# Kernel optimization log

Hardware: AMD Instinct MI355X
Metric: run time of the kernel (lower is better)

Reference implementation:

```python
import jax, jax.numpy as jnp
import numpy as np

H = 256       # lstm_hidden_size
B = 64        # batch
L = 128       # sequence length
LABEL = 128   # slot label size


def setup_inputs() -> dict:
    key = jax.random.key(0)
    ks = jax.random.split(key, 8)
    s = 1.0 / np.sqrt(H)  # torch LSTM/Linear uniform init scale
    return {
        "x": jax.random.normal(ks[0], (B, L, 2 * H), jnp.float32),
        "hi": jax.random.normal(ks[1], (B, L, 2 * H), jnp.float32),
        "W_ih": jax.random.uniform(ks[2], (4 * H, 5 * H), jnp.float32, -s, s),
        "W_hh": jax.random.uniform(ks[3], (4 * H, H), jnp.float32, -s, s),
        "b_ih": jax.random.uniform(ks[4], (4 * H,), jnp.float32, -s, s),
        "b_hh": jax.random.uniform(ks[5], (4 * H,), jnp.float32, -s, s),
        "W_fc": jax.random.uniform(ks[6], (LABEL, H), jnp.float32, -s, s),
        "b_fc": jax.random.uniform(ks[7], (LABEL,), jnp.float32, -s, s),
    }


def reference(x, hi, W_ih, W_hh, b_ih, b_hh, W_fc, b_fc):
    # dropout_rate = 0.0 -> dropout is identity.
    h_dim = W_hh.shape[1]
    bias = b_ih + b_hh  # (4H,)

    # x cat hi: (B, L, 4H) -> time-major (L, B, 4H)
    feats = jnp.transpose(jnp.concatenate([x, hi], axis=-1), (1, 0, 2))

    def cell(hc, inp):
        # PyTorch feeds (batch,1,5H) into a seq-major LSTM, so each batch
        # element is one recurrent step with batch-size 1.
        h, c = hc  # (H,), (H,)
        g = inp @ W_ih.T + h @ W_hh.T + bias  # (4H,)
        i, f, gg, o = jnp.split(g, 4)
        i = jax.nn.sigmoid(i)
        f = jax.nn.sigmoid(f)
        gg = jnp.tanh(gg)
        o = jax.nn.sigmoid(o)
        c_new = f * c + i * gg
        h_new = o * jnp.tanh(c_new)
        return (h_new, c_new), h_new

    def step(carry, x_t):
        # x_t: (B, 4H); out_prev: (B, H) = previous timestep's LSTM outputs
        h, c, out_prev = carry
        inp = jnp.concatenate([x_t, out_prev], axis=-1)  # (B, 5H)
        (h, c), outs = jax.lax.scan(cell, (h, c), inp)   # scan over batch dim
        return (h, c, outs), outs

    h0 = jnp.zeros((h_dim,), x.dtype)
    c0 = jnp.zeros((h_dim,), x.dtype)
    out0 = jnp.zeros((x.shape[0], h_dim), x.dtype)  # dec_init_out

    (_, _, _), all_out = jax.lax.scan(step, (h0, c0, out0), feats)  # (L, B, H)
    output = jnp.transpose(all_out, (1, 0, 2))  # (B, L, H)
    return output @ W_fc.T + b_fc  # (B, L, LABEL)
```

## Files before the change

kernel.cpp:

```cpp
#include <hip/hip_runtime.h>
#include <math.h>

#define H    256
#define BB   64
#define LL   128
#define LBL  128
#define NSTEP (BB*LL)
#define GDIM (4*H)
#define KDIM (4*H)
#define W5   (5*H)
#define NWG  16
#define NROW (NSTEP + 64)

typedef unsigned long long ull;

#define SW(j) ((j) + ((j) >> 4))

__global__ void k_init(ull* __restrict__ HT)
{
    const int r = blockIdx.x;
    const int e = threadIdx.x;
    HT[(ull)r * H + e] = ((ull)(unsigned)r << 32);
}

__global__ __launch_bounds__(256) void k_pre(const float* __restrict__ x,
                                             const float* __restrict__ hi,
                                             const float* __restrict__ Wih,
                                             const float* __restrict__ bih,
                                             const float* __restrict__ bhh,
                                             _Float16* __restrict__ PREh)
{
    const int nb = blockIdx.x;
    const int t  = blockIdx.y;
    const int tid = threadIdx.x;
    const int tm = tid >> 4, tn = tid & 15;

    __shared__ float As[16][68];
    __shared__ float Bs[16][68];

    const int lm  = tid >> 2;
    const int lk4 = (tid & 3) * 4;

    float acc[4][4];
#pragma unroll
    for (int i = 0; i < 4; i++)
#pragma unroll
        for (int j = 0; j < 4; j++) acc[i][j] = 0.f;

    for (int j0 = 0; j0 < KDIM; j0 += 16) {
        const int j = j0 + lk4;
        float4 av;
        if (j < 512) av = *(const float4*)(x  + ((size_t)lm * LL + t) * 512 + j);
        else         av = *(const float4*)(hi + ((size_t)lm * LL + t) * 512 + (j - 512));
        float4 bv = *(const float4*)(Wih + (size_t)(nb * 64 + lm) * W5 + j);

        __syncthreads();
        As[lk4 + 0][lm] = av.x; As[lk4 + 1][lm] = av.y;
        As[lk4 + 2][lm] = av.z; As[lk4 + 3][lm] = av.w;
        Bs[lk4 + 0][lm] = bv.x; Bs[lk4 + 1][lm] = bv.y;
        Bs[lk4 + 2][lm] = bv.z; Bs[lk4 + 3][lm] = bv.w;
        __syncthreads();

#pragma unroll
        for (int kk = 0; kk < 16; kk++) {
            float4 a = *(const float4*)&As[kk][tm << 2];
            float4 b = *(const float4*)&Bs[kk][tn << 2];
            acc[0][0] += a.x * b.x; acc[0][1] += a.x * b.y; acc[0][2] += a.x * b.z; acc[0][3] += a.x * b.w;
            acc[1][0] += a.y * b.x; acc[1][1] += a.y * b.y; acc[1][2] += a.y * b.z; acc[1][3] += a.y * b.w;
            acc[2][0] += a.z * b.x; acc[2][1] += a.z * b.y; acc[2][2] += a.z * b.z; acc[2][3] += a.z * b.w;
            acc[3][0] += a.w * b.x; acc[3][1] += a.w * b.y; acc[3][2] += a.w * b.z; acc[3][3] += a.w * b.w;
        }
    }

    const int n0 = nb * 64 + tn * 4;
    float4 b1 = *(const float4*)(bih + n0);
    float4 b2 = *(const float4*)(bhh + n0);
    const float bx = b1.x + b2.x, by = b1.y + b2.y, bz = b1.z + b2.z, bw = b1.w + b2.w;
#pragma unroll
    for (int i = 0; i < 4; i++) {
        const size_t m = (size_t)t * 64 + tm * 4 + i;
        union { _Float16 h[4]; ull u; } p;
        p.h[0] = (_Float16)(acc[i][0] + bx);
        p.h[1] = (_Float16)(acc[i][1] + by);
        p.h[2] = (_Float16)(acc[i][2] + bz);
        p.h[3] = (_Float16)(acc[i][3] + bw);
        *(ull*)(PREh + m * GDIM + n0) = p.u;
    }
}

__device__ __forceinline__ float poll_pair(const ull* p, int want, long long& budget)
{
    ull v = __hip_atomic_load(p, __ATOMIC_RELAXED, __HIP_MEMORY_SCOPE_AGENT);
    while ((int)(v >> 32) != want) {
        if (--budget < 0) break;
        v = __hip_atomic_load(p, __ATOMIC_RELAXED, __HIP_MEMORY_SCOPE_AGENT);
    }
    union { unsigned u; float f; } c; c.u = (unsigned)v;
    return c.f;
}

__global__ __launch_bounds__(1024) void k_rec(const _Float16* __restrict__ PREh,
                                              const float* __restrict__ Wih,
                                              const float* __restrict__ Whh,
                                              ull* __restrict__ HT)
{
    const int g    = blockIdx.x;
    const int tid  = threadIdx.x;
    const int w    = tid >> 6;
    const int lane = tid & 63;
    const int gate = lane >> 4;
    const int kc   = lane & 15;
    const int j_own = g * 16 + w;
    const int row   = gate * H + j_own;

    float whh[16], wo[16];
#pragma unroll
    for (int i = 0; i < 16; i++) whh[i] = Whh[(size_t)row * H + kc * 16 + i];
#pragma unroll
    for (int i = 0; i < 16; i++) wo[i]  = Wih[(size_t)row * W5 + 4 * H + kc * 16 + i];

    __shared__ float h1s[2][272];
    __shared__ float h64s[2][272];

    long long budget = 8000000LL;

    if (lane < 32) {
        const int e  = (w << 4) + (kc);
        const int rw = (lane < 16) ? 63 : 0;
        float v = poll_pair(&HT[(ull)rw * H + e], rw, budget);
        if (lane < 16) h1s[0][SW(e)] = v; else h64s[0][SW(e)] = v;
    }
    float pre_cur = (float)PREh[row];
    float c_state = 0.f;
    __syncthreads();

    for (int k = 0; k < NSTEP; ++k) {
        const int cb = k & 1, nb = cb ^ 1;

        float acc = 0.f;
        const int base = kc * 17;
#pragma unroll
        for (int q = 0; q < 4; ++q) {
            float4 a = *(const float4*)&h1s[cb][base + 4 * q];
            acc += whh[4*q+0]*a.x + whh[4*q+1]*a.y + whh[4*q+2]*a.z + whh[4*q+3]*a.w;
        }
#pragma unroll
        for (int q = 0; q < 4; ++q) {
            float4 b = *(const float4*)&h64s[cb][base + 4 * q];
            acc += wo[4*q+0]*b.x + wo[4*q+1]*b.y + wo[4*q+2]*b.z + wo[4*q+3]*b.w;
        }
        acc += __shfl_xor(acc, 1);
        acc += __shfl_xor(acc, 2);
        acc += __shfl_xor(acc, 4);
        acc += __shfl_xor(acc, 8);
        acc += pre_cur;

        float act = (gate == 2) ? tanhf(acc) : 1.f / (1.f + __expf(-acc));
        const float iv = __shfl(act,      kc);
        const float fv = __shfl(act, 16 + kc);
        const float gv = __shfl(act, 32 + kc);
        const float ov = __shfl(act, 48 + kc);
        c_state = fv * c_state + iv * gv;
        const float h = ov * tanhf(c_state);

        if (lane == 0) {
            union { float f; unsigned u; } cv; cv.f = h;
            __hip_atomic_store(&HT[(ull)(k + 64) * H + j_own],
                               ((ull)(unsigned)(k + 64) << 32) | cv.u,
                               __ATOMIC_RELAXED, __HIP_MEMORY_SCOPE_AGENT);
            h1s[nb][SW(j_own)] = h;
        }

        float pre_next = 0.f;
        if (k + 1 < NSTEP) pre_next = (float)PREh[(size_t)(k + 1) * GDIM + row];

        if (lane < 32) {
            const int e = (w << 4) + kc;
            const bool own = (lane < 16) && (w == g);
            if (!own) {
                const int rw = (lane < 16) ? (k + 64) : (k + 1);
                float v = poll_pair(&HT[(ull)rw * H + e], rw, budget);
                if (lane < 16) h1s[nb][SW(e)] = v; else h64s[nb][SW(e)] = v;
            }
        }
        pre_cur = pre_next;
        __syncthreads();
    }
}

__global__ __launch_bounds__(256) void k_fc(const ull* __restrict__ HT,
                                            const float* __restrict__ Wfc,
                                            const float* __restrict__ bfc,
                                            float* __restrict__ out)
{
    __shared__ float hl[8 * 256];
    __shared__ float wl[128 * 65];
    const int blk = blockIdx.x;
    const int tid = threadIdx.x;

#pragma unroll
    for (int kk = 0; kk < 8; kk++) {
        ull v = HT[((ull)(blk * 8 + kk + 64)) * H + tid];
        union { unsigned u; float f; } c; c.u = (unsigned)v;
        hl[kk * 256 + tid] = c.f;
    }

    const int l = tid & 127, grp = tid >> 7;
    float a0 = 0.f, a1 = 0.f, a2 = 0.f, a3 = 0.f;

    for (int c = 0; c < 4; c++) {
        __syncthreads();
        for (int m = 0; m < 32; m++) {
            const int idx = m * 256 + tid;
            const int lr = idx >> 6, jc = idx & 63;
            wl[lr * 65 + jc] = Wfc[(size_t)lr * H + c * 64 + jc];
        }
        __syncthreads();
#pragma unroll 4
        for (int jc = 0; jc < 64; jc++) {
            const float wv = wl[l * 65 + jc];
            const int hj = c * 64 + jc;
            a0 += hl[(grp * 4 + 0) * 256 + hj] * wv;
            a1 += hl[(grp * 4 + 1) * 256 + hj] * wv;
            a2 += hl[(grp * 4 + 2) * 256 + hj] * wv;
            a3 += hl[(grp * 4 + 3) * 256 + hj] * wv;
        }
    }

    const float bias = bfc[l];
    float accs[4] = {a0, a1, a2, a3};
#pragma unroll
    for (int r = 0; r < 4; r++) {
        const int k = blk * 8 + grp * 4 + r;
        const int t = k >> 6, b = k & 63;
        out[((size_t)b * LL + t) * LBL + l] = accs[r] + bias;
    }
}

extern "C" void kernel_launch(void* const* d_in, const int* in_sizes, int n_in,
                              void* d_out, int out_size, void* d_ws, size_t ws_size,
                              hipStream_t stream)
{
    const float* x   = (const float*)d_in[0];
    const float* hi  = (const float*)d_in[1];
    const float* Wih = (const float*)d_in[2];
    const float* Whh = (const float*)d_in[3];
    const float* bih = (const float*)d_in[4];
    const float* bhh = (const float*)d_in[5];
    const float* Wfc = (const float*)d_in[6];
    const float* bfc = (const float*)d_in[7];
    float* out = (float*)d_out;

    _Float16* PREh = (_Float16*)d_ws;
    ull*      HT   = (ull*)((char*)d_ws +
                            (size_t)NSTEP * GDIM * sizeof(_Float16));

    const size_t need = (size_t)NSTEP * GDIM * sizeof(_Float16)
                      + (size_t)NROW * H * sizeof(ull);
    if (ws_size < need) return;

    k_init<<<64, H, 0, stream>>>(HT);
    k_pre<<<dim3(GDIM / 64, LL), 256, 0, stream>>>(x, hi, Wih, bih, bhh, PREh);
    k_rec<<<NWG, 1024, 0, stream>>>(PREh, Wih, Whh, HT);
    k_fc<<<NSTEP / 8, 256, 0, stream>>>(HT, Wfc, bfc, out);
}
```

Measured before the change: 18.51 ms.

## Make each wave poll full hidden vectors and drop LDS exchange and barriers

Restructures the persistent recurrent kernel so each wave owns one hidden unit and computes all four gates itself. Every lane polls its four slices of the global h vector directly, and the wave reduces with a 64-wide butterfly, which removes the shared-memory h buffers and the per-step __syncthreads. The out_prev (h64) contribution plus the precomputed input is moved off the critical path, computed right after the previous step rather than inside it. Polling adds s_sleep backoff. The cost is that every wave now issues global atomic loads and a longer shuffle reduction each step, which raises memory-polling traffic.

```diff
diff --git a/kernel.cpp b/kernel.cpp
--- a/kernel.cpp
+++ b/kernel.cpp
@@ -14,8 +14,6 @@
 
 typedef unsigned long long ull;
 
-#define SW(j) ((j) + ((j) >> 4))
-
 __global__ void k_init(ull* __restrict__ HT)
 {
     const int r = blockIdx.x;
@@ -88,15 +86,39 @@
     }
 }
 
-__device__ __forceinline__ float poll_pair(const ull* p, int want, long long& budget)
-{
-    ull v = __hip_atomic_load(p, __ATOMIC_RELAXED, __HIP_MEMORY_SCOPE_AGENT);
-    while ((int)(v >> 32) != want) {
+__device__ __forceinline__ float lo_f(ull v)
+{ union { unsigned u; float f; } c; c.u = (unsigned)v; return c.f; }
+
+__device__ __forceinline__ void poll_quad(const ull* __restrict__ base, int tag,
+                                          int l, float* out, long long& budget)
+{
+    ull a0, a1, a2, a3;
+    int r = 0;
+    for (;;) {
+        a0 = __hip_atomic_load(base +       l, __ATOMIC_RELAXED, __HIP_MEMORY_SCOPE_AGENT);
+        a1 = __hip_atomic_load(base +  64 + l, __ATOMIC_RELAXED, __HIP_MEMORY_SCOPE_AGENT);
+        a2 = __hip_atomic_load(base + 128 + l, __ATOMIC_RELAXED, __HIP_MEMORY_SCOPE_AGENT);
+        a3 = __hip_atomic_load(base + 192 + l, __ATOMIC_RELAXED, __HIP_MEMORY_SCOPE_AGENT);
+        const bool ok = ((int)(a0 >> 32) == tag) & ((int)(a1 >> 32) == tag)
+                      & ((int)(a2 >> 32) == tag) & ((int)(a3 >> 32) == tag);
+        if (__all((int)ok)) break;
         if (--budget < 0) break;
-        v = __hip_atomic_load(p, __ATOMIC_RELAXED, __HIP_MEMORY_SCOPE_AGENT);
-    }
-    union { unsigned u; float f; } c; c.u = (unsigned)v;
-    return c.f;
+        ++r;
+        if (r > 16)     __builtin_amdgcn_s_sleep(8);
+        else if (r > 4) __builtin_amdgcn_s_sleep(2);
+    }
+    out[0] = lo_f(a0); out[1] = lo_f(a1); out[2] = lo_f(a2); out[3] = lo_f(a3);
+}
+
+__device__ __forceinline__ void bfly4(float& a0, float& a1, float& a2, float& a3)
+{
+#pragma unroll
+    for (int s = 1; s < 64; s <<= 1) {
+        a0 += __shfl_xor(a0, s);
+        a1 += __shfl_xor(a1, s);
+        a2 += __shfl_xor(a2, s);
+        a3 += __shfl_xor(a3, s);
+    }
 }
 
 __global__ __launch_bounds__(1024) void k_rec(const _Float16* __restrict__ PREh,
@@ -104,87 +126,85 @@
                                               const float* __restrict__ Whh,
                                               ull* __restrict__ HT)
 {
-    const int g    = blockIdx.x;
-    const int tid  = threadIdx.x;
-    const int w    = tid >> 6;
-    const int lane = tid & 63;
-    const int gate = lane >> 4;
-    const int kc   = lane & 15;
-    const int j_own = g * 16 + w;
-    const int row   = gate * H + j_own;
-
-    float whh[16], wo[16];
-#pragma unroll
-    for (int i = 0; i < 16; i++) whh[i] = Whh[(size_t)row * H + kc * 16 + i];
-#pragma unroll
-    for (int i = 0; i < 16; i++) wo[i]  = Wih[(size_t)row * W5 + 4 * H + kc * 16 + i];
-
-    __shared__ float h1s[2][272];
-    __shared__ float h64s[2][272];
-
-    long long budget = 8000000LL;
-
-    if (lane < 32) {
-        const int e  = (w << 4) + (kc);
-        const int rw = (lane < 16) ? 63 : 0;
-        float v = poll_pair(&HT[(ull)rw * H + e], rw, budget);
-        if (lane < 16) h1s[0][SW(e)] = v; else h64s[0][SW(e)] = v;
-    }
-    float pre_cur = (float)PREh[row];
-    float c_state = 0.f;
-    __syncthreads();
+    const int g   = blockIdx.x;
+    const int tid = threadIdx.x;
+    const int w   = tid >> 6;
+    const int l   = tid & 63;
+    const int j   = g * 16 + w;
+
+    float w1v[4][4], w64v[4][4];
+#pragma unroll
+    for (int g4 = 0; g4 < 4; ++g4) {
+        const int row = g4 * H + j;
+#pragma unroll
+        for (int q = 0; q < 4; ++q) {
+            w1v[g4][q]  = Whh[(size_t)row * H  + q * 64 + l];
+            w64v[g4][q] = Wih[(size_t)row * W5 + 4 * H + q * 64 + l];
+        }
+    }
+
+    long long budget = 4000000LL;
+    float h1f[4];
+    float b4[4];
+    float c = 0.f;
+
+    {
+        float h64f[4];
+        poll_quad(HT, 0, l, h64f, budget);
+        float p0 = 0.f, p1 = 0.f, p2 = 0.f, p3 = 0.f;
+#pragma unroll
+        for (int q = 0; q < 4; ++q) {
+            p0 += w64v[0][q] * h64f[q]; p1 += w64v[1][q] * h64f[q];
+            p2 += w64v[2][q] * h64f[q]; p3 += w64v[3][q] * h64f[q];
+        }
+        bfly4(p0, p1, p2, p3);
+        b4[0] = p0 + (float)PREh[0 * H + j];
+        b4[1] = p1 + (float)PREh[1 * H + j];
+        b4[2] = p2 + (float)PREh[2 * H + j];
+        b4[3] = p3 + (float)PREh[3 * H + j];
+        poll_quad(HT + (ull)63 * H, 63, l, h1f, budget);
+    }
 
     for (int k = 0; k < NSTEP; ++k) {
-        const int cb = k & 1, nb = cb ^ 1;
-
-        float acc = 0.f;
-        const int base = kc * 17;
+        float a0 = 0.f, a1 = 0.f, a2 = 0.f, a3 = 0.f;
 #pragma unroll
         for (int q = 0; q < 4; ++q) {
-            float4 a = *(const float4*)&h1s[cb][base + 4 * q];
-            acc += whh[4*q+0]*a.x + whh[4*q+1]*a.y + whh[4*q+2]*a.z + whh[4*q+3]*a.w;
-        }
-#pragma unroll
-        for (int q = 0; q < 4; ++q) {
-            float4 b = *(const float4*)&h64s[cb][base + 4 * q];
-            acc += wo[4*q+0]*b.x + wo[4*q+1]*b.y + wo[4*q+2]*b.z + wo[4*q+3]*b.w;
-        }
-        acc += __shfl_xor(acc, 1);
-        acc += __shfl_xor(acc, 2);
-        acc += __shfl_xor(acc, 4);
-        acc += __shfl_xor(acc, 8);
-        acc += pre_cur;
-
-        float act = (gate == 2) ? tanhf(acc) : 1.f / (1.f + __expf(-acc));
-        const float iv = __shfl(act,      kc);
-        const float fv = __shfl(act, 16 + kc);
-        const float gv = __shfl(act, 32 + kc);
-        const float ov = __shfl(act, 48 + kc);
-        c_state = fv * c_state + iv * gv;
-        const float h = ov * tanhf(c_state);
-
-        if (lane == 0) {
+            a0 += w1v[0][q] * h1f[q]; a1 += w1v[1][q] * h1f[q];
+            a2 += w1v[2][q] * h1f[q]; a3 += w1v[3][q] * h1f[q];
+        }
+        bfly4(a0, a1, a2, a3);
+        const float iv = 1.f / (1.f + __expf(-(a0 + b4[0])));
+        const float fv = 1.f / (1.f + __expf(-(a1 + b4[1])));
+        const float gv = tanhf(a2 + b4[2]);
+        const float ov = 1.f / (1.f + __expf(-(a3 + b4[3])));
+        c = fv * c + iv * gv;
+        const float h = ov * tanhf(c);
+
+        if (l == 0) {
             union { float f; unsigned u; } cv; cv.f = h;
-            __hip_atomic_store(&HT[(ull)(k + 64) * H + j_own],
+            __hip_atomic_store(&HT[(ull)(k + 64) * H + j],
                                ((ull)(unsigned)(k + 64) << 32) | cv.u,
                                __ATOMIC_RELAXED, __HIP_MEMORY_SCOPE_AGENT);
-            h1s[nb][SW(j_own)] = h;
-        }
-
-        float pre_next = 0.f;
-        if (k + 1 < NSTEP) pre_next = (float)PREh[(size_t)(k + 1) * GDIM + row];
-
-        if (lane < 32) {
-            const int e = (w << 4) + kc;
-            const bool own = (lane < 16) && (w == g);
-            if (!own) {
-                const int rw = (lane < 16) ? (k + 64) : (k + 1);
-                float v = poll_pair(&HT[(ull)rw * H + e], rw, budget);
-                if (lane < 16) h1s[nb][SW(e)] = v; else h64s[nb][SW(e)] = v;
+        }
+
+        if (k + 1 < NSTEP) {
+            float h64f[4];
+            poll_quad(HT + (ull)(k + 1) * H, k + 1, l, h64f, budget);
+            float p0 = 0.f, p1 = 0.f, p2 = 0.f, p3 = 0.f;
+#pragma unroll
+            for (int q = 0; q < 4; ++q) {
+                p0 += w64v[0][q] * h64f[q]; p1 += w64v[1][q] * h64f[q];
+                p2 += w64v[2][q] * h64f[q]; p3 += w64v[3][q] * h64f[q];
             }
-        }
-        pre_cur = pre_next;
-        __syncthreads();
+            bfly4(p0, p1, p2, p3);
+            const size_t pb = (size_t)(k + 1) * GDIM + j;
+            b4[0] = p0 + (float)PREh[pb];
+            b4[1] = p1 + (float)PREh[pb + H];
+            b4[2] = p2 + (float)PREh[pb + 2 * H];
+            b4[3] = p3 + (float)PREh[pb + 3 * H];
+
+            poll_quad(HT + (ull)(k + 64) * H, k + 64, l, h1f, budget);
+        }
     }
 }
 
@@ -201,8 +221,8 @@
 #pragma unroll
     for (int kk = 0; kk < 8; kk++) {
         ull v = HT[((ull)(blk * 8 + kk + 64)) * H + tid];
-        union { unsigned u; float f; } c; c.u = (unsigned)v;
-        hl[kk * 256 + tid] = c.f;
+        union { unsigned u; float f; } cc; cc.u = (unsigned)v;
+        hl[kk * 256 + tid] = cc.f;
     }
 
     const int l = tid & 127, grp = tid >> 7;
```

Result: slower. 50.86 ms (+174.8%).

## Run recurrence in single workgroup with helper blocks streaming input projections

Applied to the files above, without the earlier changes.

Drops the separate input-projection GEMM kernel and the 16-workgroup recurrence that exchanged h across workgroups every step. Now one workgroup keeps all of W_hh in registers as fp16 and runs the whole recurrence. Meanwhile 64 helper workgroups compute the W_ih projection of x, hi and the 64-step-lagged output, and publish it through a tagged ring buffer. The aim is to take the per-step cross-workgroup h polling off the serial critical path, at the cost of fp16 weights and activations in the dot products and spin-polling on the ring.

```diff
diff --git a/kernel.cpp b/kernel.cpp
--- a/kernel.cpp
+++ b/kernel.cpp
@@ -6,184 +6,200 @@
 #define LL   128
 #define LBL  128
 #define NSTEP (BB*LL)
-#define GDIM (4*H)
-#define KDIM (4*H)
 #define W5   (5*H)
-#define NWG  16
 #define NROW (NSTEP + 64)
+#define NHELP 64
+#define NPH   8
+#define RING  256
 
 typedef unsigned long long ull;
-
-#define SW(j) ((j) + ((j) >> 4))
+typedef _Float16 half2 __attribute__((ext_vector_type(2)));
+typedef _Float16 half8 __attribute__((ext_vector_type(8)));
+
+__device__ __forceinline__ float fdot2(half2 a, half2 b, float c)
+{
+#if __has_builtin(__builtin_amdgcn_fdot2)
+    return __builtin_amdgcn_fdot2(a, b, c, false);
+#else
+    return c + (float)a.x * (float)b.x + (float)a.y * (float)b.y;
+#endif
+}
+__device__ __forceinline__ float lo_f(ull v)
+{ union { unsigned u; float f; } c; c.u = (unsigned)v; return c.f; }
+__device__ __forceinline__ ull tag_pack(int tag, float f)
+{ union { float f; unsigned u; } c; c.f = f; return ((ull)(unsigned)tag << 32) | c.u; }
+__device__ __forceinline__ float sigm(float x)
+{ return __builtin_amdgcn_rcpf(1.f + __expf(-x)); }
+__device__ __forceinline__ float tanh_f(float x)
+{ float s = __expf(-2.f * x); return (1.f - s) * __builtin_amdgcn_rcpf(1.f + s); }
 
 __global__ void k_init(ull* __restrict__ HT)
 {
-    const int r = blockIdx.x;
-    const int e = threadIdx.x;
-    HT[(ull)r * H + e] = ((ull)(unsigned)r << 32);
-}
-
-__global__ __launch_bounds__(256) void k_pre(const float* __restrict__ x,
-                                             const float* __restrict__ hi,
-                                             const float* __restrict__ Wih,
-                                             const float* __restrict__ bih,
-                                             const float* __restrict__ bhh,
-                                             _Float16* __restrict__ PREh)
-{
-    const int nb = blockIdx.x;
-    const int t  = blockIdx.y;
-    const int tid = threadIdx.x;
-    const int tm = tid >> 4, tn = tid & 15;
-
-    __shared__ float As[16][68];
-    __shared__ float Bs[16][68];
-
-    const int lm  = tid >> 2;
-    const int lk4 = (tid & 3) * 4;
-
-    float acc[4][4];
-#pragma unroll
-    for (int i = 0; i < 4; i++)
-#pragma unroll
-        for (int j = 0; j < 4; j++) acc[i][j] = 0.f;
-
-    for (int j0 = 0; j0 < KDIM; j0 += 16) {
-        const int j = j0 + lk4;
-        float4 av;
-        if (j < 512) av = *(const float4*)(x  + ((size_t)lm * LL + t) * 512 + j);
-        else         av = *(const float4*)(hi + ((size_t)lm * LL + t) * 512 + (j - 512));
-        float4 bv = *(const float4*)(Wih + (size_t)(nb * 64 + lm) * W5 + j);
-
-        __syncthreads();
-        As[lk4 + 0][lm] = av.x; As[lk4 + 1][lm] = av.y;
-        As[lk4 + 2][lm] = av.z; As[lk4 + 3][lm] = av.w;
-        Bs[lk4 + 0][lm] = bv.x; Bs[lk4 + 1][lm] = bv.y;
-        Bs[lk4 + 2][lm] = bv.z; Bs[lk4 + 3][lm] = bv.w;
-        __syncthreads();
-
-#pragma unroll
-        for (int kk = 0; kk < 16; kk++) {
-            float4 a = *(const float4*)&As[kk][tm << 2];
-            float4 b = *(const float4*)&Bs[kk][tn << 2];
-            acc[0][0] += a.x * b.x; acc[0][1] += a.x * b.y; acc[0][2] += a.x * b.z; acc[0][3] += a.x * b.w;
-            acc[1][0] += a.y * b.x; acc[1][1] += a.y * b.y; acc[1][2] += a.y * b.z; acc[1][3] += a.y * b.w;
-            acc[2][0] += a.z * b.x; acc[2][1] += a.z * b.y; acc[2][2] += a.z * b.z; acc[2][3] += a.z * b.w;
-            acc[3][0] += a.w * b.x; acc[3][1] += a.w * b.y; acc[3][2] += a.w * b.z; acc[3][3] += a.w * b.w;
-        }
-    }
-
-    const int n0 = nb * 64 + tn * 4;
-    float4 b1 = *(const float4*)(bih + n0);
-    float4 b2 = *(const float4*)(bhh + n0);
-    const float bx = b1.x + b2.x, by = b1.y + b2.y, bz = b1.z + b2.z, bw = b1.w + b2.w;
-#pragma unroll
-    for (int i = 0; i < 4; i++) {
-        const size_t m = (size_t)t * 64 + tm * 4 + i;
-        union { _Float16 h[4]; ull u; } p;
-        p.h[0] = (_Float16)(acc[i][0] + bx);
-        p.h[1] = (_Float16)(acc[i][1] + by);
-        p.h[2] = (_Float16)(acc[i][2] + bz);
-        p.h[3] = (_Float16)(acc[i][3] + bw);
-        *(ull*)(PREh + m * GDIM + n0) = p.u;
-    }
-}
-
-__device__ __forceinline__ float poll_pair(const ull* p, int want, long long& budget)
-{
-    ull v = __hip_atomic_load(p, __ATOMIC_RELAXED, __HIP_MEMORY_SCOPE_AGENT);
-    while ((int)(v >> 32) != want) {
-        if (--budget < 0) break;
-        v = __hip_atomic_load(p, __ATOMIC_RELAXED, __HIP_MEMORY_SCOPE_AGENT);
-    }
-    union { unsigned u; float f; } c; c.u = (unsigned)v;
-    return c.f;
-}
-
-__global__ __launch_bounds__(1024) void k_rec(const _Float16* __restrict__ PREh,
-                                              const float* __restrict__ Wih,
-                                              const float* __restrict__ Whh,
-                                              ull* __restrict__ HT)
-{
-    const int g    = blockIdx.x;
-    const int tid  = threadIdx.x;
-    const int w    = tid >> 6;
-    const int lane = tid & 63;
-    const int gate = lane >> 4;
-    const int kc   = lane & 15;
-    const int j_own = g * 16 + w;
-    const int row   = gate * H + j_own;
-
-    float whh[16], wo[16];
-#pragma unroll
-    for (int i = 0; i < 16; i++) whh[i] = Whh[(size_t)row * H + kc * 16 + i];
-#pragma unroll
-    for (int i = 0; i < 16; i++) wo[i]  = Wih[(size_t)row * W5 + 4 * H + kc * 16 + i];
-
-    __shared__ float h1s[2][272];
-    __shared__ float h64s[2][272];
-
-    long long budget = 8000000LL;
-
-    if (lane < 32) {
-        const int e  = (w << 4) + (kc);
-        const int rw = (lane < 16) ? 63 : 0;
-        float v = poll_pair(&HT[(ull)rw * H + e], rw, budget);
-        if (lane < 16) h1s[0][SW(e)] = v; else h64s[0][SW(e)] = v;
-    }
-    float pre_cur = (float)PREh[row];
-    float c_state = 0.f;
+    HT[(ull)blockIdx.x * H + threadIdx.x] = ((ull)(unsigned)blockIdx.x << 32);
+}
+
+__global__ __launch_bounds__(512, 2)
+void k_rec(const float* __restrict__ x, const float* __restrict__ hi,
+           const float* __restrict__ Wih, const float* __restrict__ Whh,
+           const float* __restrict__ bih, const float* __restrict__ bhh,
+           ull* __restrict__ HT, ull* __restrict__ B4T)
+{
+    const int t = threadIdx.x;
+
+    if (blockIdx.x < NHELP) {
+        const int rb = blockIdx.x & 7;
+        const int ph = blockIdx.x >> 3;
+        const int r  = rb * 128 + (t >> 2);
+        const int q  = t & 3;
+
+        half2 wv[160];
+#pragma unroll
+        for (int i = 0; i < 160; ++i) {
+            float2 w = *(const float2*)&Wih[(size_t)r * W5 + q * 320 + 2 * i];
+            wv[i] = half2{(_Float16)w.x, (_Float16)w.y};
+        }
+        const float bias = bih[r] + bhh[r];
+
+        __shared__ __align__(16) _Float16 fl[1280];
+        long long budget = 200000000LL;
+
+        for (int k = ph; k < NSTEP; k += NPH) {
+            const int b = k & 63, tt = k >> 6;
+            if (t < 256) {
+                float2 v = *(const float2*)(x + ((size_t)b * LL + tt) * 512 + 2 * t);
+                fl[2 * t] = (_Float16)v.x; fl[2 * t + 1] = (_Float16)v.y;
+            } else {
+                float2 v = *(const float2*)(hi + ((size_t)b * LL + tt) * 512 + 2 * (t - 256));
+                fl[512 + 2 * (t - 256)] = (_Float16)v.x;
+                fl[513 + 2 * (t - 256)] = (_Float16)v.y;
+            }
+            if (t < 256) {
+                ull v; int rnd = 0;
+                for (;;) {
+                    v = __hip_atomic_load(&HT[(ull)k * H + t], __ATOMIC_RELAXED,
+                                          __HIP_MEMORY_SCOPE_AGENT);
+                    if ((int)(v >> 32) == k) break;
+                    if (--budget < 0) break;
+                    if (++rnd > 8) __builtin_amdgcn_s_sleep(8);
+                }
+                fl[1024 + t] = (_Float16)lo_f(v);
+            }
+            __syncthreads();
+
+            const half8* hp = (const half8*)&fl[q * 320];
+            float a0 = 0.f, a1 = 0.f, a2 = 0.f, a3 = 0.f;
+#pragma unroll
+            for (int i = 0; i < 40; ++i) {
+                half8 hv = hp[i];
+                a0 = fdot2(wv[4 * i + 0], half2{hv[0], hv[1]}, a0);
+                a1 = fdot2(wv[4 * i + 1], half2{hv[2], hv[3]}, a1);
+                a2 = fdot2(wv[4 * i + 2], half2{hv[4], hv[5]}, a2);
+                a3 = fdot2(wv[4 * i + 3], half2{hv[6], hv[7]}, a3);
+            }
+            float acc = (a0 + a1) + (a2 + a3);
+            acc += __shfl_xor(acc, 1);
+            acc += __shfl_xor(acc, 2);
+            if (q == 0)
+                __hip_atomic_store(&B4T[(ull)(k & (RING - 1)) * 1024 + r],
+                                   tag_pack(k, acc + bias),
+                                   __ATOMIC_RELAXED, __HIP_MEMORY_SCOPE_AGENT);
+            __syncthreads();
+        }
+        return;
+    }
+
+    const int q   = t & 3;
+    const int rid = t >> 2;
+    half2 wh[8][32];
+#pragma unroll
+    for (int m = 0; m < 8; ++m) {
+        const size_t row = rid + 128 * m;
+#pragma unroll
+        for (int i = 0; i < 32; ++i) {
+            float2 w = *(const float2*)&Whh[row * H + q * 64 + 2 * i];
+            wh[m][i] = half2{(_Float16)w.x, (_Float16)w.y};
+        }
+    }
+
+    __shared__ __align__(16) _Float16 h1b[2][256];
+    if (t < 256) h1b[0][t] = (_Float16)0.f;
     __syncthreads();
 
+    long long budget = 200000000LL;
+    float c0 = 0.f, c1 = 0.f;
+
+    ull b4v[8];
+#pragma unroll
+    for (int m = 0; m < 8; ++m)
+        b4v[m] = __hip_atomic_load(&B4T[rid + 128 * m], __ATOMIC_RELAXED,
+                                   __HIP_MEMORY_SCOPE_AGENT);
+
     for (int k = 0; k < NSTEP; ++k) {
-        const int cb = k & 1, nb = cb ^ 1;
-
-        float acc = 0.f;
-        const int base = kc * 17;
-#pragma unroll
-        for (int q = 0; q < 4; ++q) {
-            float4 a = *(const float4*)&h1s[cb][base + 4 * q];
-            acc += whh[4*q+0]*a.x + whh[4*q+1]*a.y + whh[4*q+2]*a.z + whh[4*q+3]*a.w;
-        }
-#pragma unroll
-        for (int q = 0; q < 4; ++q) {
-            float4 b = *(const float4*)&h64s[cb][base + 4 * q];
-            acc += wo[4*q+0]*b.x + wo[4*q+1]*b.y + wo[4*q+2]*b.z + wo[4*q+3]*b.w;
-        }
-        acc += __shfl_xor(acc, 1);
-        acc += __shfl_xor(acc, 2);
-        acc += __shfl_xor(acc, 4);
-        acc += __shfl_xor(acc, 8);
-        acc += pre_cur;
-
-        float act = (gate == 2) ? tanhf(acc) : 1.f / (1.f + __expf(-acc));
-        const float iv = __shfl(act,      kc);
-        const float fv = __shfl(act, 16 + kc);
-        const float gv = __shfl(act, 32 + kc);
-        const float ov = __shfl(act, 48 + kc);
-        c_state = fv * c_state + iv * gv;
-        const float h = ov * tanhf(c_state);
-
-        if (lane == 0) {
-            union { float f; unsigned u; } cv; cv.f = h;
-            __hip_atomic_store(&HT[(ull)(k + 64) * H + j_own],
-                               ((ull)(unsigned)(k + 64) << 32) | cv.u,
+        const int cb = k & 1;
+
+        {
+            int rnd = 0;
+            for (;;) {
+                bool ok = true;
+#pragma unroll
+                for (int m = 0; m < 8; ++m) ok &= ((int)(b4v[m] >> 32) == k);
+                if (__all((int)ok)) break;
+                if (--budget < 0) break;
+                if (++rnd > 4) __builtin_amdgcn_s_sleep(1);
+                const ull* bp = &B4T[(ull)(k & (RING - 1)) * 1024 + rid];
+#pragma unroll
+                for (int m = 0; m < 8; ++m)
+                    b4v[m] = __hip_atomic_load(bp + 128 * m, __ATOMIC_RELAXED,
+                                               __HIP_MEMORY_SCOPE_AGENT);
+            }
+        }
+
+        const half8* hp = (const half8*)&h1b[cb][q * 64];
+        float sA[8] = {0,0,0,0,0,0,0,0}, sB[8] = {0,0,0,0,0,0,0,0};
+#pragma unroll
+        for (int i = 0; i < 8; ++i) {
+            half8 hv = hp[i];
+            half2 p0 = half2{hv[0], hv[1]}, p1 = half2{hv[2], hv[3]};
+            half2 p2 = half2{hv[4], hv[5]}, p3 = half2{hv[6], hv[7]};
+#pragma unroll
+            for (int m = 0; m < 8; ++m) {
+                sA[m] = fdot2(wh[m][4 * i + 0], p0, sA[m]);
+                sB[m] = fdot2(wh[m][4 * i + 1], p1, sB[m]);
+                sA[m] = fdot2(wh[m][4 * i + 2], p2, sA[m]);
+                sB[m] = fdot2(wh[m][4 * i + 3], p3, sB[m]);
+            }
+        }
+        float g[8];
+#pragma unroll
+        for (int m = 0; m < 8; ++m) {
+            float s = sA[m] + sB[m];
+            s += __shfl_xor(s, 1);
+            s += __shfl_xor(s, 2);
+            g[m] = s + lo_f(b4v[m]);
+        }
+        const float i0 = sigm(g[0]), f0 = sigm(g[2]), q0 = tanh_f(g[4]), o0 = sigm(g[6]);
+        const float i1 = sigm(g[1]), f1 = sigm(g[3]), q1 = tanh_f(g[5]), o1 = sigm(g[7]);
+        c0 = f0 * c0 + i0 * q0;  const float h0 = o0 * tanh_f(c0);
+        c1 = f1 * c1 + i1 * q1;  const float h1v = o1 * tanh_f(c1);
+
+        if (q == 0) {
+            ull* hp_ = &HT[(ull)(k + 64) * H + rid];
+            __hip_atomic_store(hp_,       tag_pack(k + 64, h0),
                                __ATOMIC_RELAXED, __HIP_MEMORY_SCOPE_AGENT);
-            h1s[nb][SW(j_own)] = h;
-        }
-
-        float pre_next = 0.f;
-        if (k + 1 < NSTEP) pre_next = (float)PREh[(size_t)(k + 1) * GDIM + row];
-
-        if (lane < 32) {
-            const int e = (w << 4) + kc;
-            const bool own = (lane < 16) && (w == g);
-            if (!own) {
-                const int rw = (lane < 16) ? (k + 64) : (k + 1);
-                float v = poll_pair(&HT[(ull)rw * H + e], rw, budget);
-                if (lane < 16) h1s[nb][SW(e)] = v; else h64s[nb][SW(e)] = v;
-            }
-        }
-        pre_cur = pre_next;
+            __hip_atomic_store(hp_ + 128, tag_pack(k + 64, h1v),
+                               __ATOMIC_RELAXED, __HIP_MEMORY_SCOPE_AGENT);
+        } else if (q == 1) {
+            h1b[cb ^ 1][rid]       = (_Float16)h0;
+            h1b[cb ^ 1][rid + 128] = (_Float16)h1v;
+        }
+
+        if (k + 1 < NSTEP) {
+            const ull* bp = &B4T[(ull)((k + 1) & (RING - 1)) * 1024 + rid];
+#pragma unroll
+            for (int m = 0; m < 8; ++m)
+                b4v[m] = __hip_atomic_load(bp + 128 * m, __ATOMIC_RELAXED,
+                                           __HIP_MEMORY_SCOPE_AGENT);
+        }
         __syncthreads();
     }
 }
@@ -199,11 +215,8 @@
     const int tid = threadIdx.x;
 
 #pragma unroll
-    for (int kk = 0; kk < 8; kk++) {
-        ull v = HT[((ull)(blk * 8 + kk + 64)) * H + tid];
-        union { unsigned u; float f; } c; c.u = (unsigned)v;
-        hl[kk * 256 + tid] = c.f;
-    }
+    for (int kk = 0; kk < 8; kk++)
+        hl[kk * 256 + tid] = lo_f(HT[((ull)(blk * 8 + kk + 64)) * H + tid]);
 
     const int l = tid & 127, grp = tid >> 7;
     float a0 = 0.f, a1 = 0.f, a2 = 0.f, a3 = 0.f;
@@ -232,8 +245,8 @@
 #pragma unroll
     for (int r = 0; r < 4; r++) {
         const int k = blk * 8 + grp * 4 + r;
-        const int t = k >> 6, b = k & 63;
-        out[((size_t)b * LL + t) * LBL + l] = accs[r] + bias;
+        const int tt = k >> 6, b = k & 63;
+        out[((size_t)b * LL + tt) * LBL + l] = accs[r] + bias;
     }
 }
 
@@ -251,16 +264,13 @@
     const float* bfc = (const float*)d_in[7];
     float* out = (float*)d_out;
 
-    _Float16* PREh = (_Float16*)d_ws;
-    ull*      HT   = (ull*)((char*)d_ws +
-                            (size_t)NSTEP * GDIM * sizeof(_Float16));
-
-    const size_t need = (size_t)NSTEP * GDIM * sizeof(_Float16)
-                      + (size_t)NROW * H * sizeof(ull);
+    ull* HT  = (ull*)d_ws;
+    ull* B4T = HT + (size_t)NROW * H;
+
+    const size_t need = ((size_t)NROW * H + (size_t)RING * 1024) * sizeof(ull);
     if (ws_size < need) return;
 
     k_init<<<64, H, 0, stream>>>(HT);
-    k_pre<<<dim3(GDIM / 64, LL), 256, 0, stream>>>(x, hi, Wih, bih, bhh, PREh);
-    k_rec<<<NWG, 1024, 0, stream>>>(PREh, Wih, Whh, HT);
+    k_rec<<<NHELP + 1, 512, 0, stream>>>(x, hi, Wih, Whh, bih, bhh, HT, B4T);
     k_fc<<<NSTEP / 8, 256, 0, stream>>>(HT, Wfc, bfc, out);
 }
```

Result: slower. 44.70 ms (+141.5%).
